# Optimization experiments

Hardware: AMD Instinct MI355X
Metric: run time of the kernel (lower is better)

## Reference

```python
import jax, jax.numpy as jnp
import numpy as np

B, L, D, H = 2, 2048, 512, 8
HS = D // H          # head_size = 64
BLOCK = 2048         # block_size
EPS = 1e-5


def setup_inputs() -> dict:
    key = jax.random.key(0)
    ks = jax.random.split(key, 8)
    s = 0.02
    x = jax.random.normal(ks[0], (B, L, D), jnp.float32)
    mask = jnp.triu(jnp.ones((1, 1, L, L), bool), k=1)  # causal: True above diag
    wq = jax.random.normal(ks[1], (D, D), jnp.float32) * s
    wk = jax.random.normal(ks[2], (D, D), jnp.float32) * s
    wv = jax.random.normal(ks[3], (D, D), jnp.float32) * s
    wo = jax.random.normal(ks[4], (D, D), jnp.float32) * s
    Er = jax.random.normal(ks[5], (H, BLOCK, HS), jnp.float32)
    bq = jnp.zeros((D,), jnp.float32)
    bk = jnp.zeros((D,), jnp.float32)
    bv = jnp.zeros((D,), jnp.float32)
    bo = jnp.zeros((D,), jnp.float32)
    ln_g = jnp.ones((D,), jnp.float32)
    ln_b = jnp.zeros((D,), jnp.float32)
    return dict(x=x, mask=mask, ln_g=ln_g, ln_b=ln_b, wq=wq, bq=bq,
                wk=wk, bk=bk, wv=wv, bv=bv, wo=wo, bo=bo, Er=Er)


def _skew(qe):
    # qe: [B, H, L, L] -> pad last dim on the left, reshape trick, drop first row
    padded = jnp.pad(qe, ((0, 0), (0, 0), (0, 0), (1, 0)))
    b, h, l, l1 = padded.shape
    return padded.reshape(b, h, l1, l)[:, :, 1:, :]


def reference(x, mask, ln_g, ln_b, wq, bq, wk, bk, wv, bv, wo, bo, Er):
    l = x.shape[1]
    # LayerNorm
    mu = jnp.mean(x, axis=-1, keepdims=True)
    var = jnp.mean((x - mu) ** 2, axis=-1, keepdims=True)
    hn = (x - mu) / jnp.sqrt(var + EPS) * ln_g + ln_b
    # QKV: [B, H, L, HS]
    q = (hn @ wq.T + bq).reshape(-1, l, H, HS).transpose(0, 2, 1, 3)
    k = (hn @ wk.T + bk).reshape(-1, l, H, HS).transpose(0, 2, 1, 3)
    v = (hn @ wv.T + bv).reshape(-1, l, H, HS).transpose(0, 2, 1, 3)
    # relative position bias via skew
    Ers = Er[:, BLOCK - l:, :]                       # [H, l, HS]
    QEr = jnp.einsum('bhld,hmd->bhlm', q, Ers)       # [B, H, L, L]
    SRel = _skew(QEr)
    # scaled dot-product scores
    w = jnp.einsum('bhld,bhmd->bhlm', q, k) * (HS ** -0.5)
    w = jnp.where(mask, -jnp.inf, w)
    SRel = jnp.where(mask, -jnp.inf, SRel)
    w = jax.nn.softmax(w + SRel, axis=-1)            # dropout omitted (eval mode)
    out = jnp.einsum('bhlm,bhmd->bhld', w, v)
    out = out.transpose(0, 2, 1, 3).reshape(-1, l, D)
    return out @ wo.T + bo
```

## Files before the change

kernel.cpp:

```cpp
#include <hip/hip_runtime.h>

#define LSEQ 2048
#define DIM 512
#define NH 8
#define HS 64

typedef __attribute__((ext_vector_type(8))) short short8;
typedef __attribute__((ext_vector_type(4))) float f32x4;

__device__ inline unsigned short f2bf(float f) {
  union { float f; unsigned u; } a; a.f = f;
  unsigned r = a.u + 0x7FFFu + ((a.u >> 16) & 1u);
  return (unsigned short)(r >> 16);
}
__device__ inline float bf2f(unsigned short h) {
  union { unsigned u; float f; } a; a.u = ((unsigned)h) << 16;
  return a.f;
}
__device__ inline unsigned cvtpk(float lo, float hi) {
  unsigned r;
  asm("v_cvt_pk_bf16_f32 %0, %1, %2" : "=v"(r) : "v"(lo), "v"(hi));
  return r;
}
__device__ inline float fexp2(float x) {
  float r;
  asm("v_exp_f32 %0, %1" : "=v"(r) : "v"(x));
  return r;
}

__device__ inline f32x4 mfma_bf16(short8 a, short8 b, f32x4 c) {
  return __builtin_amdgcn_mfma_f32_16x16x32_bf16(a, b, c, 0, 0, 0);
}

__device__ inline short8 ld8(const unsigned short* p) {
  return *reinterpret_cast<const short8*>(p);
}

#define GLLDS(SRC, DST) __builtin_amdgcn_global_load_lds( \
    (const __attribute__((address_space(1))) void*)(SRC), \
    (__attribute__((address_space(3))) void*)(DST), 16, 0, 0)

__device__ inline int frag_idx(int row, int d) {
  return (((row >> 4) * 2 + (d >> 5)) << 9) + (((row & 15) + ((d >> 3) & 3) * 16) << 3) + (d & 7);
}

__global__ __launch_bounds__(256) void cvt_all_kernel(
    const float* __restrict__ wq, const float* __restrict__ wk,
    const float* __restrict__ wv, const float* __restrict__ wo,
    const float* __restrict__ Er,
    unsigned short* __restrict__ wqb, unsigned short* __restrict__ wkb,
    unsigned short* __restrict__ wvb, unsigned short* __restrict__ wob,
    unsigned short* __restrict__ erb) {
  int b = blockIdx.x;
  if (b < 1024) {
    const float* src; unsigned short* dst; int off;
    if (b < 256)       { src = wq; dst = wqb; off = b; }
    else if (b < 512)  { src = wk; dst = wkb; off = b - 256; }
    else if (b < 768)  { src = wv; dst = wvb; off = b - 512; }
    else               { src = wo; dst = wob; off = b - 768; }
    int i = (off * 256 + threadIdx.x) * 4;
    float4 v = *reinterpret_cast<const float4*>(src + i);
    unsigned lo = (unsigned)f2bf(v.x) | ((unsigned)f2bf(v.y) << 16);
    unsigned hi = (unsigned)f2bf(v.z) | ((unsigned)f2bf(v.w) << 16);
    uint2 pk; pk.x = lo; pk.y = hi;
    *reinterpret_cast<uint2*>(dst + i) = pk;
  } else {
    const float scl = 1.4426950408889634f;
    int i = ((b - 1024) * 256 + threadIdx.x) * 4;
    int hh = i >> 17;
    int rem = i & ((1 << 17) - 1);
    int er = rem >> 6, d = rem & 63;
    float4 v = *reinterpret_cast<const float4*>(Er + i);
    unsigned lo = (unsigned)f2bf(v.x * scl) | ((unsigned)f2bf(v.y * scl) << 16);
    unsigned hi = (unsigned)f2bf(v.z * scl) | ((unsigned)f2bf(v.w * scl) << 16);
    uint2 pk; pk.x = lo; pk.y = hi;
    unsigned short* dst = erb + (size_t)hh * LSEQ * HS + frag_idx(er, d);
    *reinterpret_cast<uint2*>(dst) = pk;
  }
}

__global__ __launch_bounds__(256) void ln_kernel(const float* __restrict__ x,
    const float* __restrict__ g, const float* __restrict__ bta,
    unsigned short* __restrict__ hn) {
  int lane = threadIdx.x & 63, w = threadIdx.x >> 6;
  int row = blockIdx.x * 4 + w;
  const float4* xr = reinterpret_cast<const float4*>(x + (size_t)row * DIM);
  float4 a = xr[2 * lane], c = xr[2 * lane + 1];
  float s = a.x + a.y + a.z + a.w + c.x + c.y + c.z + c.w;
  float sq = a.x * a.x + a.y * a.y + a.z * a.z + a.w * a.w +
             c.x * c.x + c.y * c.y + c.z * c.z + c.w * c.w;
#pragma unroll
  for (int off = 1; off < 64; off <<= 1) {
    s += __shfl_xor(s, off);
    sq += __shfl_xor(sq, off);
  }
  float mu = s * (1.f / DIM);
  float var = sq * (1.f / DIM) - mu * mu;
  float rstd = rsqrtf(var + 1e-5f);
  float4 g0 = reinterpret_cast<const float4*>(g)[2 * lane];
  float4 g1 = reinterpret_cast<const float4*>(g)[2 * lane + 1];
  float4 b0 = reinterpret_cast<const float4*>(bta)[2 * lane];
  float4 b1 = reinterpret_cast<const float4*>(bta)[2 * lane + 1];
  uint4 o;
  o.x = (unsigned)f2bf((a.x - mu) * rstd * g0.x + b0.x) |
        ((unsigned)f2bf((a.y - mu) * rstd * g0.y + b0.y) << 16);
  o.y = (unsigned)f2bf((a.z - mu) * rstd * g0.z + b0.z) |
        ((unsigned)f2bf((a.w - mu) * rstd * g0.w + b0.w) << 16);
  o.z = (unsigned)f2bf((c.x - mu) * rstd * g1.x + b1.x) |
        ((unsigned)f2bf((c.y - mu) * rstd * g1.y + b1.y) << 16);
  o.w = (unsigned)f2bf((c.z - mu) * rstd * g1.z + b1.z) |
        ((unsigned)f2bf((c.w - mu) * rstd * g1.w + b1.w) << 16);
  reinterpret_cast<uint4*>(hn)[(size_t)row * 64 + lane] = o;
}

__global__ __launch_bounds__(256, 3) void qkv_kernel(const unsigned short* __restrict__ hn,
    const unsigned short* __restrict__ wqb, const unsigned short* __restrict__ wkb,
    const unsigned short* __restrict__ wvb,
    const float* __restrict__ bq, const float* __restrict__ bk, const float* __restrict__ bv,
    unsigned short* __restrict__ qo, unsigned short* __restrict__ ko,
    unsigned short* __restrict__ vT) {
  __shared__ unsigned short As[3][128 * 32];
  __shared__ unsigned short Bs[3][128 * 32];
  int tid = threadIdx.x, lane = tid & 63, w = tid >> 6;
  int mcol = lane & 15, grp = lane >> 4;
  int l4 = lane >> 2, lql = lane & 3;
  int bid = blockIdx.x;
  int mat = bid >> 7;
  int rem = bid & 127;
  int m0 = (rem >> 2) << 7;
  int n0 = (rem & 3) << 7;
  const unsigned short* W = (mat == 0) ? wqb : (mat == 1) ? wkb : wvb;
  const float* bias = (mat == 0) ? bq : (mat == 1) ? bk : bv;
  float scl = (mat == 1) ? 0.18033688011112042f : 1.f;
  int wr = w >> 1, wc = w & 1;

  f32x4 acc[4][4];
#pragma unroll
  for (int i = 0; i < 4; ++i)
#pragma unroll
    for (int j = 0; j < 4; ++j) acc[i][j] = (f32x4){0.f, 0.f, 0.f, 0.f};

#pragma unroll
  for (int j = 0; j < 2; ++j) {
    int row = 32 * w + 16 * j + l4;
    GLLDS(hn + (size_t)(m0 + row) * DIM + lql * 8, &As[0][(32 * w + 16 * j) * 32]);
    GLLDS(W + (size_t)(n0 + row) * DIM + lql * 8, &Bs[0][(32 * w + 16 * j) * 32]);
  }
  for (int kk = 0; kk < 16; ++kk) {
    int buf = kk % 3;
    if (kk < 15) {
      int nbuf = (kk + 1) % 3;
      int k0 = (kk + 1) * 32;
#pragma unroll
      for (int j = 0; j < 2; ++j) {
        int row = 32 * w + 16 * j + l4;
        GLLDS(hn + (size_t)(m0 + row) * DIM + k0 + lql * 8, &As[nbuf][(32 * w + 16 * j) * 32]);
        GLLDS(W + (size_t)(n0 + row) * DIM + k0 + lql * 8, &Bs[nbuf][(32 * w + 16 * j) * 32]);
      }
      asm volatile("s_waitcnt vmcnt(4)\n\ts_barrier" ::: "memory");
    } else {
      asm volatile("s_waitcnt vmcnt(0)\n\ts_barrier" ::: "memory");
    }
    const unsigned short* AL = As[buf];
    const unsigned short* BL = Bs[buf];
    short8 af[4], bf[4];
#pragma unroll
    for (int f = 0; f < 4; ++f) {
      af[f] = ld8(&AL[(wr * 64 + f * 16 + mcol) * 32 + grp * 8]);
      bf[f] = ld8(&BL[(wc * 64 + f * 16 + mcol) * 32 + grp * 8]);
    }
#pragma unroll
    for (int fi = 0; fi < 4; ++fi)
#pragma unroll
      for (int fj = 0; fj < 4; ++fj)
        acc[fi][fj] = mfma_bf16(af[fi], bf[fj], acc[fi][fj]);
  }
#pragma unroll
  for (int fj = 0; fj < 4; ++fj) {
    int n = n0 + wc * 64 + fj * 16 + mcol;
    int hh = n >> 6, d = n & 63;
    float bsv = bias[n];
#pragma unroll
    for (int fi = 0; fi < 4; ++fi) {
#pragma unroll
      for (int r = 0; r < 4; ++r) {
        int m = m0 + wr * 64 + fi * 16 + 4 * grp + r;
        float val = (acc[fi][fj][r] + bsv) * scl;
        int b = m >> 11, l = m & (LSEQ - 1);
        unsigned short hv = f2bf(val);
        size_t base = (size_t)(b * NH + hh) * HS * LSEQ;
        if (mat == 2) {
          int idx = (((l >> 5) * 4 + (d >> 4)) * 64 + ((l >> 3) & 3) * 16 + (d & 15)) * 8 + (l & 7);
          vT[base + idx] = hv;
        } else if (mat == 1) {
          ko[base + frag_idx(l, d)] = hv;
        } else {
          qo[((size_t)(b * NH + hh) * LSEQ + l) * HS + d] = hv;
        }
      }
    }
  }
}

__global__ __launch_bounds__(256, 3) void attn_kernel(const unsigned short* __restrict__ q,
    const unsigned short* __restrict__ k, const unsigned short* __restrict__ vT,
    const unsigned short* __restrict__ erb, char* __restrict__ partials) {
  __shared__ float Uall[4][32 * 100];
  int tid = threadIdx.x, lane = tid & 63, w = tid >> 6;
  int mcol = lane & 15, grp = lane >> 4;
  float* U = Uall[w];

  int bid = blockIdx.x;
  int xcd = bid & 7, s = bid >> 3;
  int hi2 = (s >= 40) ? 1 : 0;
  int bh = xcd + 8 * hi2;
  int bu = s - 40 * hi2;
  int ubp = 159 - (bu * 4 + w);
  int T, cc;
  if (ubp < 16)      { T = ubp; cc = 0; }
  else if (ubp < 48) { int idx = ubp - 16; T = 16 + (idx >> 1); cc = idx & 1; }
  else if (ubp < 96) { int idx = ubp - 48; int t3 = idx / 3; T = 32 + t3; cc = idx - 3 * t3; }
  else               { int idx = ubp - 96; T = 48 + (idx >> 2); cc = idx & 3; }
  int qi0w = T << 5;
  int c0 = cc << 9;
  int kend = min(c0 + 512, qi0w + 32);
  int nkb = (kend - c0 + 63) >> 6;
  int h = bh & 7;

  const unsigned short* Qb = q + (size_t)bh * LSEQ * HS;
  const unsigned short* Kb = k + (size_t)bh * LSEQ * HS;
  const unsigned short* Vb = vT + (size_t)bh * HS * LSEQ;
  const unsigned short* Eb = erb + (size_t)h * LSEQ * HS;

  short8 qf[2][2];
#pragma unroll
  for (int mg = 0; mg < 2; ++mg) {
    qf[mg][0] = ld8(Qb + (size_t)(qi0w + 16 * mg + mcol) * HS + 8 * grp);
    qf[mg][1] = ld8(Qb + (size_t)(qi0w + 16 * mg + mcol) * HS + 32 + 8 * grp);
  }

  f32x4 o[2][4];
#pragma unroll
  for (int mg = 0; mg < 2; ++mg)
#pragma unroll
    for (int i = 0; i < 4; ++i) o[mg][i] = (f32x4){0.f, 0.f, 0.f, 0.f};
  float la0 = 0.f, la1 = 0.f;
  int srcA = mcol | ((grp & 1) << 5);
  int srcB = srcA + 16;
  bool hi = (grp >= 2);
  int loff = lane * 8;

  for (int kb = 0; kb < nkb; ++kb) {
    int kj0 = c0 + (kb << 6);
    int E0 = 2016 - qi0w + kj0;
    int g0 = E0 >> 4;
    short8 ef[12];
#pragma unroll
    for (int jt = 0; jt < 6; ++jt) {
      int gg = g0 + jt;
      if (gg > 127) gg = 127;
      ef[2 * jt]     = ld8(Eb + (size_t)(gg * 2) * 512 + loff);
      ef[2 * jt + 1] = ld8(Eb + (size_t)(gg * 2 + 1) * 512 + loff);
    }
#pragma unroll
    for (int jt = 0; jt < 6; ++jt) {
      f32x4 u0 = (f32x4){0.f, 0.f, 0.f, 0.f};
      u0 = mfma_bf16(ef[2 * jt], qf[0][0], u0);
      u0 = mfma_bf16(ef[2 * jt + 1], qf[0][1], u0);
      f32x4 u1 = (f32x4){0.f, 0.f, 0.f, 0.f};
      u1 = mfma_bf16(ef[2 * jt], qf[1][0], u1);
      u1 = mfma_bf16(ef[2 * jt + 1], qf[1][1], u1);
      *reinterpret_cast<f32x4*>(&U[mcol * 100 + 16 * jt + 4 * grp]) = u0;
      *reinterpret_cast<f32x4*>(&U[(mcol + 16) * 100 + 16 * jt + 4 * grp]) = u1;
    }
    short8 kf[8];
#pragma unroll
    for (int t = 0; t < 4; ++t) {
      int blk = ((kj0 >> 4) + t) * 2;
      kf[2 * t]     = ld8(Kb + (size_t)blk * 512 + loff);
      kf[2 * t + 1] = ld8(Kb + (size_t)(blk + 1) * 512 + loff);
    }
    f32x4 stv[2][4];
#pragma unroll
    for (int mg = 0; mg < 2; ++mg)
#pragma unroll
      for (int t = 0; t < 4; ++t) {
        f32x4 a_ = (f32x4){0.f, 0.f, 0.f, 0.f};
        a_ = mfma_bf16(kf[2 * t], qf[mg][0], a_);
        a_ = mfma_bf16(kf[2 * t + 1], qf[mg][1], a_);
        stv[mg][t] = a_;
      }
    float lt[2][4][4];
#pragma unroll
    for (int mg = 0; mg < 2; ++mg) {
      int m = mcol + 16 * mg;
      bool am = (kj0 + 63) > (qi0w + 16 * mg);
      if (am) {
#pragma unroll
        for (int t = 0; t < 4; ++t) {
          const float* up = &U[m * 100 + 16 * t + 4 * grp - m + 31];
#pragma unroll
          for (int r = 0; r < 4; ++r) {
            int n = 16 * t + 4 * grp + r;
            float val = stv[mg][t][r] + up[r];
            val = (kj0 + n > qi0w + m) ? -1e30f : val;
            float p_ = fexp2(val);
            lt[mg][t][r] = p_;
            if (mg == 0) la0 += p_; else la1 += p_;
          }
        }
      } else {
#pragma unroll
        for (int t = 0; t < 4; ++t) {
          const float* up = &U[m * 100 + 16 * t + 4 * grp - m + 31];
#pragma unroll
          for (int r = 0; r < 4; ++r) {
            float p_ = fexp2(stv[mg][t][r] + up[r]);
            lt[mg][t][r] = p_;
            if (mg == 0) la0 += p_; else la1 += p_;
          }
        }
      }
    }
    short8 vf[8];
#pragma unroll
    for (int s2 = 0; s2 < 2; ++s2)
#pragma unroll
      for (int dt = 0; dt < 4; ++dt)
        vf[s2 * 4 + dt] = ld8(Vb + (size_t)(((kj0 >> 5) + s2) * 4 + dt) * 512 + loff);
#pragma unroll
    for (int mg = 0; mg < 2; ++mg) {
      unsigned w0[4], w1[4];
#pragma unroll
      for (int t = 0; t < 4; ++t) {
        w0[t] = cvtpk(lt[mg][t][0], lt[mg][t][1]);
        w1[t] = cvtpk(lt[mg][t][2], lt[mg][t][3]);
      }
#pragma unroll
      for (int s2 = 0; s2 < 2; ++s2) {
        unsigned y0a = (unsigned)__shfl((int)w0[2 * s2], srcA);
        unsigned y0b = (unsigned)__shfl((int)w0[2 * s2 + 1], srcA);
        unsigned y1a = (unsigned)__shfl((int)w1[2 * s2], srcA);
        unsigned y1b = (unsigned)__shfl((int)w1[2 * s2 + 1], srcA);
        unsigned y2a = (unsigned)__shfl((int)w0[2 * s2], srcB);
        unsigned y2b = (unsigned)__shfl((int)w0[2 * s2 + 1], srcB);
        unsigned y3a = (unsigned)__shfl((int)w1[2 * s2], srcB);
        unsigned y3b = (unsigned)__shfl((int)w1[2 * s2 + 1], srcB);
        union { unsigned u4[4]; short8 s8; } pu;
        pu.u4[0] = hi ? y0b : y0a;
        pu.u4[1] = hi ? y1b : y1a;
        pu.u4[2] = hi ? y2b : y2a;
        pu.u4[3] = hi ? y3b : y3a;
#pragma unroll
        for (int dt = 0; dt < 4; ++dt)
          o[mg][dt] = mfma_bf16(vf[s2 * 4 + dt], pu.s8, o[mg][dt]);
      }
    }
  }

  la0 += __shfl_xor(la0, 16);
  la0 += __shfl_xor(la0, 32);
  la1 += __shfl_xor(la1, 16);
  la1 += __shfl_xor(la1, 32);

  int pid = bh * 160 + ubp;
  char* pb = partials + (size_t)pid * 4224;
  unsigned* Ob = (unsigned*)pb;
#pragma unroll
  for (int mg = 0; mg < 2; ++mg)
#pragma unroll
    for (int dt = 0; dt < 4; ++dt) {
      Ob[(mcol + 16 * mg) * 32 + dt * 8 + grp * 2]     = cvtpk(o[mg][dt][0], o[mg][dt][1]);
      Ob[(mcol + 16 * mg) * 32 + dt * 8 + grp * 2 + 1] = cvtpk(o[mg][dt][2], o[mg][dt][3]);
    }
  if (grp == 0) {
    ((float*)(pb + 4096))[mcol]      = la0;
    ((float*)(pb + 4096))[mcol + 16] = la1;
  }
}

__global__ __launch_bounds__(256) void merge_kernel(const char* __restrict__ partials,
    unsigned short* __restrict__ attT) {
  int lane = threadIdx.x & 63, w = threadIdx.x >> 6;
  int bid = blockIdx.x;
  int xcd = bid & 7, s = bid >> 3;
  int hi2 = (s >= 16) ? 1 : 0;
  int bh = xcd + 8 * hi2;
  int T = (s - 16 * hi2) * 4 + w;
  int g = T >> 4;
  int start = (g == 0) ? 0 : (g == 1) ? 16 : (g == 2) ? 48 : 96;
  int nch = g + 1;
  int base_u = bh * 160 + start + (T & 15) * nch;
  int row = lane & 31, dh = lane >> 5;
  float acc[32];
#pragma unroll
  for (int j = 0; j < 32; ++j) acc[j] = 0.f;
  float lsum = 0.f;
  for (int c = 0; c < nch; ++c) {
    const char* pb = partials + (size_t)(base_u + c) * 4224;
    lsum += ((const float*)(pb + 4096))[row];
    const unsigned short* Op = (const unsigned short*)pb + row * 64 + dh * 32;
#pragma unroll
    for (int jj = 0; jj < 4; ++jj) {
      short8 v = ld8(Op + jj * 8);
#pragma unroll
      for (int e = 0; e < 8; ++e)
        acc[jj * 8 + e] += bf2f((unsigned short)v[e]);
    }
  }
  float inv = 1.f / lsum;
  int b = bh >> 3, h = bh & 7;
  unsigned short* dst = attT + ((size_t)(b * LSEQ) + T * 32 + row) * DIM + h * HS + dh * 32;
  union { unsigned short us[32]; short8 s8[4]; } ou;
#pragma unroll
  for (int j = 0; j < 32; ++j) ou.us[j] = f2bf(acc[j] * inv);
#pragma unroll
  for (int jj = 0; jj < 4; ++jj)
    *reinterpret_cast<short8*>(dst + jj * 8) = ou.s8[jj];
}

__global__ __launch_bounds__(256, 3) void out_kernel(const unsigned short* __restrict__ attT,
    const unsigned short* __restrict__ wob, const float* __restrict__ bo,
    float* __restrict__ out) {
  __shared__ unsigned short As[3][128 * 32];
  __shared__ unsigned short Bs[3][64 * 32];
  int tid = threadIdx.x, lane = tid & 63, w = tid >> 6;
  int mcol = lane & 15, grp = lane >> 4;
  int l4 = lane >> 2, lql = lane & 3;
  int bid = blockIdx.x;
  int m0 = (bid >> 3) << 7;
  int n0 = (bid & 7) << 6;
  int wr = w >> 1, wc = w & 1;

  f32x4 acc[4][2];
#pragma unroll
  for (int i = 0; i < 4; ++i)
#pragma unroll
    for (int j = 0; j < 2; ++j) acc[i][j] = (f32x4){0.f, 0.f, 0.f, 0.f};

#pragma unroll
  for (int j = 0; j < 2; ++j) {
    int row = 32 * w + 16 * j + l4;
    GLLDS(attT + (size_t)(m0 + row) * DIM + lql * 8, &As[0][(32 * w + 16 * j) * 32]);
  }
  {
    int row = 16 * w + l4;
    GLLDS(wob + (size_t)(n0 + row) * DIM + lql * 8, &Bs[0][(16 * w) * 32]);
  }
  for (int kk = 0; kk < 16; ++kk) {
    int buf = kk % 3;
    if (kk < 15) {
      int nbuf = (kk + 1) % 3;
      int k0 = (kk + 1) * 32;
#pragma unroll
      for (int j = 0; j < 2; ++j) {
        int row = 32 * w + 16 * j + l4;
        GLLDS(attT + (size_t)(m0 + row) * DIM + k0 + lql * 8, &As[nbuf][(32 * w + 16 * j) * 32]);
      }
      {
        int row = 16 * w + l4;
        GLLDS(wob + (size_t)(n0 + row) * DIM + k0 + lql * 8, &Bs[nbuf][(16 * w) * 32]);
      }
      asm volatile("s_waitcnt vmcnt(3)\n\ts_barrier" ::: "memory");
    } else {
      asm volatile("s_waitcnt vmcnt(0)\n\ts_barrier" ::: "memory");
    }
    const unsigned short* AL = As[buf];
    const unsigned short* BL = Bs[buf];
    short8 af[4], bf[2];
#pragma unroll
    for (int f = 0; f < 4; ++f)
      af[f] = ld8(&AL[(wr * 64 + f * 16 + mcol) * 32 + grp * 8]);
#pragma unroll
    for (int f = 0; f < 2; ++f)
      bf[f] = ld8(&BL[(wc * 32 + f * 16 + mcol) * 32 + grp * 8]);
#pragma unroll
    for (int fi = 0; fi < 4; ++fi)
#pragma unroll
      for (int fj = 0; fj < 2; ++fj)
        acc[fi][fj] = mfma_bf16(af[fi], bf[fj], acc[fi][fj]);
  }
#pragma unroll
  for (int fj = 0; fj < 2; ++fj) {
    int n = n0 + wc * 32 + fj * 16 + mcol;
    float bsv = bo[n];
#pragma unroll
    for (int fi = 0; fi < 4; ++fi) {
#pragma unroll
      for (int r = 0; r < 4; ++r) {
        int m = m0 + wr * 64 + fi * 16 + 4 * grp + r;
        out[(size_t)m * DIM + n] = acc[fi][fj][r] + bsv;
      }
    }
  }
}

extern "C" void kernel_launch(void* const* d_in, const int* in_sizes, int n_in,
                              void* d_out, int out_size, void* d_ws, size_t ws_size,
                              hipStream_t stream) {
  const float* x    = (const float*)d_in[0];
  const float* ln_g = (const float*)d_in[2];
  const float* ln_b = (const float*)d_in[3];
  const float* wq   = (const float*)d_in[4];
  const float* bq   = (const float*)d_in[5];
  const float* wk   = (const float*)d_in[6];
  const float* bk   = (const float*)d_in[7];
  const float* wv   = (const float*)d_in[8];
  const float* bv   = (const float*)d_in[9];
  const float* wo   = (const float*)d_in[10];
  const float* bo   = (const float*)d_in[11];
  const float* Er   = (const float*)d_in[12];
  float* out = (float*)d_out;

  char* ws = (char*)d_ws;
  unsigned short* hn   = (unsigned short*)(ws);
  unsigned short* qb   = (unsigned short*)(ws + (4u << 20));
  unsigned short* kb   = (unsigned short*)(ws + (8u << 20));
  unsigned short* vT   = (unsigned short*)(ws + (12u << 20));
  unsigned short* erb  = (unsigned short*)(ws + (16u << 20));
  unsigned short* attT = (unsigned short*)(ws + (18u << 20));
  unsigned short* wqb  = (unsigned short*)(ws + (22u << 20));
  unsigned short* wkb  = wqb + 512 * 512;
  unsigned short* wvb  = wkb + 512 * 512;
  unsigned short* wob  = wvb + 512 * 512;
  char* partials       = ws + (24u << 20);

  cvt_all_kernel<<<2048, 256, 0, stream>>>(wq, wk, wv, wo, Er, wqb, wkb, wvb, wob, erb);
  ln_kernel<<<1024, 256, 0, stream>>>(x, ln_g, ln_b, hn);
  qkv_kernel<<<384, 256, 0, stream>>>(hn, wqb, wkb, wvb, bq, bk, bv, qb, kb, vT);
  attn_kernel<<<640, 256, 0, stream>>>(qb, kb, vT, erb, partials);
  merge_kernel<<<256, 256, 0, stream>>>(partials, attT);
  out_kernel<<<256, 256, 0, stream>>>(attT, wob, bo, out);
}
```

Before: 76.57 us.

## Fuse LN into prep kernel, write single-chunk attention rows directly, reuse Er fragments

Merges the layernorm launch into the weight/Er conversion kernel, which removes one kernel launch. Attention units whose rows have only one key chunk now normalize and write their output straight into attT, so the merge kernel runs fewer blocks. In the attention loop, Er fragments that overlap between iterations are carried forward instead of reloaded, and K loads are issued before the Er MFMAs to hide latency. This adds some register pressure and control-flow divergence in the epilogue.

After: 73.92 us. 3.5% less time.

```diff
diff --git a/kernel.cpp b/kernel.cpp
--- a/kernel.cpp
+++ b/kernel.cpp
@@ -44,13 +44,14 @@
   return (((row >> 4) * 2 + (d >> 5)) << 9) + (((row & 15) + ((d >> 3) & 3) * 16) << 3) + (d & 7);
 }
 
-__global__ __launch_bounds__(256) void cvt_all_kernel(
+__global__ __launch_bounds__(256) void prep_kernel(
     const float* __restrict__ wq, const float* __restrict__ wk,
     const float* __restrict__ wv, const float* __restrict__ wo,
-    const float* __restrict__ Er,
+    const float* __restrict__ Er, const float* __restrict__ x,
+    const float* __restrict__ ln_g, const float* __restrict__ ln_b,
     unsigned short* __restrict__ wqb, unsigned short* __restrict__ wkb,
     unsigned short* __restrict__ wvb, unsigned short* __restrict__ wob,
-    unsigned short* __restrict__ erb) {
+    unsigned short* __restrict__ erb, unsigned short* __restrict__ hn) {
   int b = blockIdx.x;
   if (b < 1024) {
     const float* src; unsigned short* dst; int off;
@@ -64,7 +65,7 @@
     unsigned hi = (unsigned)f2bf(v.z) | ((unsigned)f2bf(v.w) << 16);
     uint2 pk; pk.x = lo; pk.y = hi;
     *reinterpret_cast<uint2*>(dst + i) = pk;
-  } else {
+  } else if (b < 2048) {
     const float scl = 1.4426950408889634f;
     int i = ((b - 1024) * 256 + threadIdx.x) * 4;
     int hh = i >> 17;
@@ -76,41 +77,37 @@
     uint2 pk; pk.x = lo; pk.y = hi;
     unsigned short* dst = erb + (size_t)hh * LSEQ * HS + frag_idx(er, d);
     *reinterpret_cast<uint2*>(dst) = pk;
-  }
-}
-
-__global__ __launch_bounds__(256) void ln_kernel(const float* __restrict__ x,
-    const float* __restrict__ g, const float* __restrict__ bta,
-    unsigned short* __restrict__ hn) {
-  int lane = threadIdx.x & 63, w = threadIdx.x >> 6;
-  int row = blockIdx.x * 4 + w;
-  const float4* xr = reinterpret_cast<const float4*>(x + (size_t)row * DIM);
-  float4 a = xr[2 * lane], c = xr[2 * lane + 1];
-  float s = a.x + a.y + a.z + a.w + c.x + c.y + c.z + c.w;
-  float sq = a.x * a.x + a.y * a.y + a.z * a.z + a.w * a.w +
-             c.x * c.x + c.y * c.y + c.z * c.z + c.w * c.w;
-#pragma unroll
-  for (int off = 1; off < 64; off <<= 1) {
-    s += __shfl_xor(s, off);
-    sq += __shfl_xor(sq, off);
-  }
-  float mu = s * (1.f / DIM);
-  float var = sq * (1.f / DIM) - mu * mu;
-  float rstd = rsqrtf(var + 1e-5f);
-  float4 g0 = reinterpret_cast<const float4*>(g)[2 * lane];
-  float4 g1 = reinterpret_cast<const float4*>(g)[2 * lane + 1];
-  float4 b0 = reinterpret_cast<const float4*>(bta)[2 * lane];
-  float4 b1 = reinterpret_cast<const float4*>(bta)[2 * lane + 1];
-  uint4 o;
-  o.x = (unsigned)f2bf((a.x - mu) * rstd * g0.x + b0.x) |
-        ((unsigned)f2bf((a.y - mu) * rstd * g0.y + b0.y) << 16);
-  o.y = (unsigned)f2bf((a.z - mu) * rstd * g0.z + b0.z) |
-        ((unsigned)f2bf((a.w - mu) * rstd * g0.w + b0.w) << 16);
-  o.z = (unsigned)f2bf((c.x - mu) * rstd * g1.x + b1.x) |
-        ((unsigned)f2bf((c.y - mu) * rstd * g1.y + b1.y) << 16);
-  o.w = (unsigned)f2bf((c.z - mu) * rstd * g1.z + b1.z) |
-        ((unsigned)f2bf((c.w - mu) * rstd * g1.w + b1.w) << 16);
-  reinterpret_cast<uint4*>(hn)[(size_t)row * 64 + lane] = o;
+  } else {
+    int lane = threadIdx.x & 63, w = threadIdx.x >> 6;
+    int row = (b - 2048) * 4 + w;
+    const float4* xr = reinterpret_cast<const float4*>(x + (size_t)row * DIM);
+    float4 a = xr[2 * lane], c = xr[2 * lane + 1];
+    float s = a.x + a.y + a.z + a.w + c.x + c.y + c.z + c.w;
+    float sq = a.x * a.x + a.y * a.y + a.z * a.z + a.w * a.w +
+               c.x * c.x + c.y * c.y + c.z * c.z + c.w * c.w;
+#pragma unroll
+    for (int off = 1; off < 64; off <<= 1) {
+      s += __shfl_xor(s, off);
+      sq += __shfl_xor(sq, off);
+    }
+    float mu = s * (1.f / DIM);
+    float var = sq * (1.f / DIM) - mu * mu;
+    float rstd = rsqrtf(var + 1e-5f);
+    float4 g0 = reinterpret_cast<const float4*>(ln_g)[2 * lane];
+    float4 g1 = reinterpret_cast<const float4*>(ln_g)[2 * lane + 1];
+    float4 b0 = reinterpret_cast<const float4*>(ln_b)[2 * lane];
+    float4 b1 = reinterpret_cast<const float4*>(ln_b)[2 * lane + 1];
+    uint4 o;
+    o.x = (unsigned)f2bf((a.x - mu) * rstd * g0.x + b0.x) |
+          ((unsigned)f2bf((a.y - mu) * rstd * g0.y + b0.y) << 16);
+    o.y = (unsigned)f2bf((a.z - mu) * rstd * g0.z + b0.z) |
+          ((unsigned)f2bf((a.w - mu) * rstd * g0.w + b0.w) << 16);
+    o.z = (unsigned)f2bf((c.x - mu) * rstd * g1.x + b1.x) |
+          ((unsigned)f2bf((c.y - mu) * rstd * g1.y + b1.y) << 16);
+    o.w = (unsigned)f2bf((c.z - mu) * rstd * g1.z + b1.z) |
+          ((unsigned)f2bf((c.w - mu) * rstd * g1.w + b1.w) << 16);
+    reinterpret_cast<uint4*>(hn)[(size_t)row * 64 + lane] = o;
+  }
 }
 
 __global__ __launch_bounds__(256, 3) void qkv_kernel(const unsigned short* __restrict__ hn,
@@ -204,7 +201,8 @@
 
 __global__ __launch_bounds__(256, 3) void attn_kernel(const unsigned short* __restrict__ q,
     const unsigned short* __restrict__ k, const unsigned short* __restrict__ vT,
-    const unsigned short* __restrict__ erb, char* __restrict__ partials) {
+    const unsigned short* __restrict__ erb, char* __restrict__ partials,
+    unsigned short* __restrict__ attT) {
   __shared__ float Uall[4][32 * 100];
   int tid = threadIdx.x, lane = tid & 63, w = tid >> 6;
   int mcol = lane & 15, grp = lane >> 4;
@@ -250,17 +248,32 @@
   bool hi = (grp >= 2);
   int loff = lane * 8;
 
+  int g0i = (2016 - qi0w + c0) >> 4;
+  short8 ef[12];
+  {
+    int ga = min(g0i, 127), gb = min(g0i + 1, 127);
+    ef[0] = ld8(Eb + (size_t)(ga * 2) * 512 + loff);
+    ef[1] = ld8(Eb + (size_t)(ga * 2 + 1) * 512 + loff);
+    ef[2] = ld8(Eb + (size_t)(gb * 2) * 512 + loff);
+    ef[3] = ld8(Eb + (size_t)(gb * 2 + 1) * 512 + loff);
+  }
+
   for (int kb = 0; kb < nkb; ++kb) {
     int kj0 = c0 + (kb << 6);
-    int E0 = 2016 - qi0w + kj0;
-    int g0 = E0 >> 4;
-    short8 ef[12];
-#pragma unroll
-    for (int jt = 0; jt < 6; ++jt) {
+    int g0 = g0i + 4 * kb;
+#pragma unroll
+    for (int jt = 2; jt < 6; ++jt) {
       int gg = g0 + jt;
       if (gg > 127) gg = 127;
-      ef[2 * jt]     = ld8(Eb + (size_t)(gg * 2) * 512 + loff);
+      ef[2 * jt] = ld8(Eb + (size_t)(gg * 2) * 512 + loff);
       ef[2 * jt + 1] = ld8(Eb + (size_t)(gg * 2 + 1) * 512 + loff);
+    }
+    short8 kf[8];
+#pragma unroll
+    for (int t = 0; t < 4; ++t) {
+      int blk = ((kj0 >> 4) + t) * 2;
+      kf[2 * t]     = ld8(Kb + (size_t)blk * 512 + loff);
+      kf[2 * t + 1] = ld8(Kb + (size_t)(blk + 1) * 512 + loff);
     }
 #pragma unroll
     for (int jt = 0; jt < 6; ++jt) {
@@ -272,13 +285,6 @@
       u1 = mfma_bf16(ef[2 * jt + 1], qf[1][1], u1);
       *reinterpret_cast<f32x4*>(&U[mcol * 100 + 16 * jt + 4 * grp]) = u0;
       *reinterpret_cast<f32x4*>(&U[(mcol + 16) * 100 + 16 * jt + 4 * grp]) = u1;
-    }
-    short8 kf[8];
-#pragma unroll
-    for (int t = 0; t < 4; ++t) {
-      int blk = ((kj0 >> 4) + t) * 2;
-      kf[2 * t]     = ld8(Kb + (size_t)blk * 512 + loff);
-      kf[2 * t + 1] = ld8(Kb + (size_t)(blk + 1) * 512 + loff);
     }
     f32x4 stv[2][4];
 #pragma unroll
@@ -356,6 +362,7 @@
           o[mg][dt] = mfma_bf16(vf[s2 * 4 + dt], pu.s8, o[mg][dt]);
       }
     }
+    ef[0] = ef[8]; ef[1] = ef[9]; ef[2] = ef[10]; ef[3] = ef[11];
   }
 
   la0 += __shfl_xor(la0, 16);
@@ -363,19 +370,36 @@
   la1 += __shfl_xor(la1, 16);
   la1 += __shfl_xor(la1, 32);
 
-  int pid = bh * 160 + ubp;
-  char* pb = partials + (size_t)pid * 4224;
-  unsigned* Ob = (unsigned*)pb;
-#pragma unroll
-  for (int mg = 0; mg < 2; ++mg)
+  if (ubp < 16) {
+    float inv0 = 1.f / la0, inv1 = 1.f / la1;
+    int b2 = bh >> 3;
+    size_t rb0 = ((size_t)(b2 * LSEQ) + qi0w + mcol) * DIM + h * HS;
+    size_t rb1 = rb0 + (size_t)16 * DIM;
 #pragma unroll
     for (int dt = 0; dt < 4; ++dt) {
-      Ob[(mcol + 16 * mg) * 32 + dt * 8 + grp * 2]     = cvtpk(o[mg][dt][0], o[mg][dt][1]);
-      Ob[(mcol + 16 * mg) * 32 + dt * 8 + grp * 2 + 1] = cvtpk(o[mg][dt][2], o[mg][dt][3]);
-    }
-  if (grp == 0) {
-    ((float*)(pb + 4096))[mcol]      = la0;
-    ((float*)(pb + 4096))[mcol + 16] = la1;
+      uint2 p0, p1;
+      p0.x = cvtpk(o[0][dt][0] * inv0, o[0][dt][1] * inv0);
+      p0.y = cvtpk(o[0][dt][2] * inv0, o[0][dt][3] * inv0);
+      p1.x = cvtpk(o[1][dt][0] * inv1, o[1][dt][1] * inv1);
+      p1.y = cvtpk(o[1][dt][2] * inv1, o[1][dt][3] * inv1);
+      *reinterpret_cast<uint2*>(attT + rb0 + dt * 16 + 4 * grp) = p0;
+      *reinterpret_cast<uint2*>(attT + rb1 + dt * 16 + 4 * grp) = p1;
+    }
+  } else {
+    int pid = bh * 160 + ubp;
+    char* pb = partials + (size_t)pid * 4224;
+    unsigned* Ob = (unsigned*)pb;
+#pragma unroll
+    for (int mg = 0; mg < 2; ++mg)
+#pragma unroll
+      for (int dt = 0; dt < 4; ++dt) {
+        Ob[(mcol + 16 * mg) * 32 + dt * 8 + grp * 2]     = cvtpk(o[mg][dt][0], o[mg][dt][1]);
+        Ob[(mcol + 16 * mg) * 32 + dt * 8 + grp * 2 + 1] = cvtpk(o[mg][dt][2], o[mg][dt][3]);
+      }
+    if (grp == 0) {
+      ((float*)(pb + 4096))[mcol]      = la0;
+      ((float*)(pb + 4096))[mcol + 16] = la1;
+    }
   }
 }
 
@@ -384,11 +408,11 @@
   int lane = threadIdx.x & 63, w = threadIdx.x >> 6;
   int bid = blockIdx.x;
   int xcd = bid & 7, s = bid >> 3;
-  int hi2 = (s >= 16) ? 1 : 0;
+  int hi2 = (s >= 12) ? 1 : 0;
   int bh = xcd + 8 * hi2;
-  int T = (s - 16 * hi2) * 4 + w;
+  int T = 16 + (s - 12 * hi2) * 4 + w;
   int g = T >> 4;
-  int start = (g == 0) ? 0 : (g == 1) ? 16 : (g == 2) ? 48 : 96;
+  int start = (g == 1) ? 16 : (g == 2) ? 48 : 96;
   int nch = g + 1;
   int base_u = bh * 160 + start + (T & 15) * nch;
   int row = lane & 31, dh = lane >> 5;
@@ -525,10 +549,10 @@
   unsigned short* wob  = wvb + 512 * 512;
   char* partials       = ws + (24u << 20);
 
-  cvt_all_kernel<<<2048, 256, 0, stream>>>(wq, wk, wv, wo, Er, wqb, wkb, wvb, wob, erb);
-  ln_kernel<<<1024, 256, 0, stream>>>(x, ln_g, ln_b, hn);
+  prep_kernel<<<3072, 256, 0, stream>>>(wq, wk, wv, wo, Er, x, ln_g, ln_b,
+                                        wqb, wkb, wvb, wob, erb, hn);
   qkv_kernel<<<384, 256, 0, stream>>>(hn, wqb, wkb, wvb, bq, bk, bv, qb, kb, vT);
-  attn_kernel<<<640, 256, 0, stream>>>(qb, kb, vT, erb, partials);
-  merge_kernel<<<256, 256, 0, stream>>>(partials, attT);
+  attn_kernel<<<640, 256, 0, stream>>>(qb, kb, vT, erb, partials, attT);
+  merge_kernel<<<192, 256, 0, stream>>>(partials, attT);
   out_kernel<<<256, 256, 0, stream>>>(attT, wob, bo, out);
 }
```
